# Kernel tuning notes

Measured on AMD Instinct MI355X. Metric: run time of the kernel, lower is better.

The kernel has to match this reference:

```python
import jax, jax.numpy as jnp
import numpy as np

N_SVC = 100000
N_EP = 100000
E = 300000
D = 128
H = 128


def _sage(x_src, x_dst, edge_index, Wl, bl, Wr, n_dst):
    """PyG SAGEConv default: mean neighbor aggr, lin_l(aggr) + lin_r(x_dst)."""
    src, dst = edge_index[0], edge_index[1]
    msg = x_src[src]                                        # [E, D] gather
    sums = jax.ops.segment_sum(msg, dst, num_segments=n_dst)  # [n_dst, D]
    cnt = jax.ops.segment_sum(jnp.ones((msg.shape[0], 1), msg.dtype), dst,
                              num_segments=n_dst)             # [n_dst, 1]
    mean = sums / jnp.maximum(cnt, 1.0)
    return mean @ Wl.T + bl + x_dst @ Wr.T                  # [n_dst, H]


def setup_inputs() -> dict:
    key = jax.random.key(0)
    ks = jax.random.split(key, 16)
    scale = 1.0 / np.sqrt(D)
    inp = {
        "x_service": jax.random.normal(ks[0], (N_SVC, D), jnp.float32),
        "x_endpoint": jax.random.normal(ks[1], (N_EP, D), jnp.float32),
        "ei_calls": jax.random.randint(ks[2], (2, E), 0, N_SVC),   # svc -> svc
        "ei_has": jax.random.randint(ks[3], (2, E), 0, N_SVC),     # svc -> ep (dst < N_EP too)
        "ei_belongs": jax.random.randint(ks[4], (2, E), 0, N_EP),  # ep -> svc
        "Wl_calls": jax.random.normal(ks[5], (H, D), jnp.float32) * scale,
        "bl_calls": jnp.zeros((H,), jnp.float32),
        "Wr_calls": jax.random.normal(ks[6], (H, D), jnp.float32) * scale,
        "Wl_has": jax.random.normal(ks[7], (H, D), jnp.float32) * scale,
        "bl_has": jnp.zeros((H,), jnp.float32),
        "Wr_has": jax.random.normal(ks[8], (H, D), jnp.float32) * scale,
        "Wl_belongs": jax.random.normal(ks[9], (H, D), jnp.float32) * scale,
        "bl_belongs": jnp.zeros((H,), jnp.float32),
        "Wr_belongs": jax.random.normal(ks[10], (H, D), jnp.float32) * scale,
    }
    return inp


def reference(x_service, x_endpoint, ei_calls, ei_has, ei_belongs,
              Wl_calls, bl_calls, Wr_calls,
              Wl_has, bl_has, Wr_has,
              Wl_belongs, bl_belongs, Wr_belongs):
    # edge type (service, calls, service) -> service output
    out_calls = _sage(x_service, x_service, ei_calls, Wl_calls, bl_calls, Wr_calls, N_SVC)
    # edge type (endpoint, belongs, service) -> service output
    out_belongs = _sage(x_endpoint, x_service, ei_belongs, Wl_belongs, bl_belongs, Wr_belongs, N_SVC)
    # edge type (service, has, endpoint) -> endpoint output
    out_has = _sage(x_service, x_endpoint, ei_has, Wl_has, bl_has, Wr_has, N_EP)
    # HeteroConv aggr='sum': sum per destination node type
    out_service = out_calls + out_belongs
    out_endpoint = out_has
    return out_service, out_endpoint
```

## Files before the change

kernel.cpp:

```cpp
#include <hip/hip_runtime.h>

#define DF 128
#define CAP 24

typedef __bf16 bf16x8 __attribute__((ext_vector_type(8)));
typedef float f32x4 __attribute__((ext_vector_type(4)));
typedef unsigned short ushort8v __attribute__((ext_vector_type(8)));

__device__ __forceinline__ unsigned short f2bf(float f) {
    union { float f; unsigned int u; } v; v.f = f;
    unsigned int r = v.u + 0x7FFFu + ((v.u >> 16) & 1u);
    return (unsigned short)(r >> 16);
}
__device__ __forceinline__ float bf2f(unsigned short u) {
    union { unsigned int u; float f; } v; v.u = ((unsigned int)u) << 16;
    return v.f;
}

__global__ __launch_bounds__(256)
void prep_kernel(
                 const int* __restrict__ ei_calls, int E1,
                 const int* __restrict__ ei_belongs, int E2,
                 const int* __restrict__ ei_has, int E3,
                 int* __restrict__ cnt, int* __restrict__ slots,
                 const float* __restrict__ x_service,
                 const float* __restrict__ x_endpoint,
                 unsigned short* __restrict__ A_svc,
                 unsigned short* __restrict__ A_ep,
                 int n_svc, int n_ep,
                 const float* __restrict__ Wl_calls, const float* __restrict__ Wr_calls,
                 const float* __restrict__ Wl_belongs, const float* __restrict__ Wr_belongs,
                 const float* __restrict__ Wl_has, const float* __restrict__ Wr_has,
                 const float* __restrict__ bl_calls, const float* __restrict__ bl_belongs,
                 const float* __restrict__ bl_has,
                 unsigned short* __restrict__ Bp_svc, unsigned short* __restrict__ Bp_ep,
                 float* __restrict__ bias_svc, float* __restrict__ bias_ep,
                 int B_fill, int B_pack)
{
    int b = blockIdx.x;

    if (b < B_fill) {
        int e = b * 256 + threadIdx.x;
        int Etot = E1 + E2 + E3;
        if (e >= Etot) return;
        int s, d, base;
        if (e < E1)           { s = ei_calls[e]; d = ei_calls[E1 + e]; base = 0; }
        else if (e < E1 + E2) { int el = e - E1; s = ei_belongs[el]; d = ei_belongs[E2 + el]; base = n_svc; }
        else                  { int el = e - E1 - E2; s = ei_has[el]; d = ei_has[E3 + el]; base = 2 * n_svc; }
        int g = base + d;
        int pos = atomicAdd(cnt + g, 1);
        if (pos < CAP) slots[(size_t)g * CAP + pos] = s;
        return;
    }
    b -= B_fill;

    if (b < B_pack) {
        int t = b * 256 + threadIdx.x;
        const int SV = 12 * 8 * 64 * 8;
        const int EPN = 8 * 8 * 64 * 8;
        if (t < SV) {
            int j = t & 7, lane = (t >> 3) & 63, ct = (t >> 9) & 7, kt = t >> 12;
            int k = kt * 32 + (lane >> 4) * 8 + j;
            int n = ct * 16 + (lane & 15);
            float v;
            if (k < 128)       v = Wl_calls[n * DF + k];
            else if (k < 256)  v = Wl_belongs[n * DF + (k - 128)];
            else               v = Wr_calls[n * DF + (k - 256)] + Wr_belongs[n * DF + (k - 256)];
            Bp_svc[t] = f2bf(v);
        } else if (t < SV + EPN) {
            int t2 = t - SV;
            int j = t2 & 7, lane = (t2 >> 3) & 63, ct = (t2 >> 9) & 7, kt = t2 >> 12;
            int k = kt * 32 + (lane >> 4) * 8 + j;
            int n = ct * 16 + (lane & 15);
            float v = (k < 128) ? Wl_has[n * DF + k] : Wr_has[n * DF + (k - 128)];
            Bp_ep[t2] = f2bf(v);
        }
        if (t < 128) bias_svc[t] = bl_calls[t] + bl_belongs[t];
        else if (t < 256) bias_ep[t - 128] = bl_has[t - 128];
        return;
    }
    b -= B_pack;

    int tid = b * 256 + threadIdx.x;
    int node = tid >> 5;
    int c4 = (tid & 31) << 2;
    if (node < n_svc) {
        float4 v = *reinterpret_cast<const float4*>(x_service + (size_t)node * DF + c4);
        ushort4 o; o.x = f2bf(v.x); o.y = f2bf(v.y); o.z = f2bf(v.z); o.w = f2bf(v.w);
        *reinterpret_cast<ushort4*>(A_svc + (size_t)node * 384 + 256 + c4) = o;
    } else if (node < n_svc + n_ep) {
        int ne = node - n_svc;
        float4 v = *reinterpret_cast<const float4*>(x_endpoint + (size_t)ne * DF + c4);
        ushort4 o; o.x = f2bf(v.x); o.y = f2bf(v.y); o.z = f2bf(v.z); o.w = f2bf(v.w);
        *reinterpret_cast<ushort4*>(A_ep + (size_t)ne * 256 + 128 + c4) = o;
    }
}

__global__ __launch_bounds__(256)
void aggregate_kernel(unsigned short* __restrict__ A_svc,
                      unsigned short* __restrict__ A_ep,
                      const int* __restrict__ cnt,
                      const int* __restrict__ slots,
                      int n_svc, int n_ep)
{
    int tid = blockIdx.x * blockDim.x + threadIdx.x;
    int g = tid >> 4;
    int NT = 2 * n_svc + n_ep;
    if (g >= NT) return;
    int c8 = (tid & 15) << 3;

    const unsigned short* src_base;
    size_t src_stride, src_off;
    unsigned short* outp;
    if (g < n_svc) {
        src_base = A_svc; src_stride = 384; src_off = 256;
        outp = A_svc + (size_t)g * 384 + c8;
    } else if (g < 2 * n_svc) {
        src_base = A_ep; src_stride = 256; src_off = 128;
        outp = A_svc + (size_t)(g - n_svc) * 384 + 128 + c8;
    } else {
        src_base = A_svc; src_stride = 384; src_off = 256;
        outp = A_ep + (size_t)(g - 2 * n_svc) * 256 + c8;
    }

    int deg = cnt[g];
    if (deg > CAP) deg = CAP;
    const int* sp = slots + (size_t)g * CAP;

    float acc[8];
#pragma unroll
    for (int q = 0; q < 8; ++q) acc[q] = 0.f;

    for (int i0 = 0; i0 < deg; i0 += 8) {
        int idx[8];
#pragma unroll
        for (int j = 0; j < 8; ++j) {
            int ii = i0 + j;
            if (ii > deg - 1) ii = deg - 1;
            idx[j] = sp[ii];
        }
        ushort8v v[8];
#pragma unroll
        for (int j = 0; j < 8; ++j)
            v[j] = *reinterpret_cast<const ushort8v*>(
                src_base + (size_t)idx[j] * src_stride + src_off + c8);
        int nv = deg - i0;
#pragma unroll
        for (int j = 0; j < 8; ++j) {
            if (j < nv) {
#pragma unroll
                for (int q = 0; q < 8; ++q) acc[q] += bf2f(v[j][q]);
            }
        }
    }

    float inv = 1.0f / (float)max(deg, 1);
    ushort8v o;
#pragma unroll
    for (int q = 0; q < 8; ++q) o[q] = f2bf(acc[q] * inv);
    *reinterpret_cast<ushort8v*>(outp) = o;
}

template <int KSTEPS>
__global__ __launch_bounds__(256)
void mfma_gemm(const unsigned short* __restrict__ A,
               const unsigned short* __restrict__ Bpack,
               const float* __restrict__ bias,
               float* __restrict__ out, int M)
{
    const int lane = threadIdx.x & 63;
    const int wave = threadIdx.x >> 6;
    const int quad = lane >> 4;
    const int lc = lane & 15;
    const int row0 = blockIdx.x * 128 + wave * 32;
    int m0 = row0 + lc;
    int m1 = row0 + 16 + lc;
    if (m0 > M - 1) m0 = M - 1;
    if (m1 > M - 1) m1 = M - 1;
    const int K = KSTEPS * 32;
    const unsigned short* Ap0 = A + (size_t)m0 * K + quad * 8;
    const unsigned short* Ap1 = A + (size_t)m1 * K + quad * 8;
    const unsigned short* Bp = Bpack + lane * 8;

    f32x4 acc0[8], acc1[8];
#pragma unroll
    for (int ct = 0; ct < 8; ++ct) {
        acc0[ct] = (f32x4){0.f, 0.f, 0.f, 0.f};
        acc1[ct] = (f32x4){0.f, 0.f, 0.f, 0.f};
    }

#pragma unroll
    for (int kt = 0; kt < KSTEPS; ++kt) {
        bf16x8 af0 = *reinterpret_cast<const bf16x8*>(Ap0 + kt * 32);
        bf16x8 af1 = *reinterpret_cast<const bf16x8*>(Ap1 + kt * 32);
        const unsigned short* b = Bp + (size_t)kt * 8 * 512;
#pragma unroll
        for (int ct = 0; ct < 8; ++ct) {
            bf16x8 bf = *reinterpret_cast<const bf16x8*>(b + ct * 512);
            acc0[ct] = __builtin_amdgcn_mfma_f32_16x16x32_bf16(af0, bf, acc0[ct], 0, 0, 0);
            acc1[ct] = __builtin_amdgcn_mfma_f32_16x16x32_bf16(af1, bf, acc1[ct], 0, 0, 0);
        }
    }

    float bc[8];
#pragma unroll
    for (int ct = 0; ct < 8; ++ct) bc[ct] = bias[ct * 16 + lc];

#pragma unroll
    for (int half = 0; half < 2; ++half) {
        int orow0 = row0 + half * 16 + quad * 4;
        f32x4* accp = half ? acc1 : acc0;
#pragma unroll
        for (int r = 0; r < 4; ++r) {
            int orow = orow0 + r;
            if (orow < M) {
                float* op = out + (size_t)orow * DF + lc;
#pragma unroll
                for (int ct = 0; ct < 8; ++ct) op[ct * 16] = accp[ct][r] + bc[ct];
            }
        }
    }
}

extern "C" void kernel_launch(void* const* d_in, const int* in_sizes, int n_in,
                              void* d_out, int out_size, void* d_ws, size_t ws_size,
                              hipStream_t stream)
{
    const float* x_service  = (const float*)d_in[0];
    const float* x_endpoint = (const float*)d_in[1];
    const int*   ei_calls   = (const int*)d_in[2];
    const int*   ei_has     = (const int*)d_in[3];
    const int*   ei_belongs = (const int*)d_in[4];
    const float* Wl_calls   = (const float*)d_in[5];
    const float* bl_calls   = (const float*)d_in[6];
    const float* Wr_calls   = (const float*)d_in[7];
    const float* Wl_has     = (const float*)d_in[8];
    const float* bl_has     = (const float*)d_in[9];
    const float* Wr_has     = (const float*)d_in[10];
    const float* Wl_belongs = (const float*)d_in[11];
    const float* bl_belongs = (const float*)d_in[12];
    const float* Wr_belongs = (const float*)d_in[13];

    const int n_svc = in_sizes[0] / DF;
    const int n_ep  = in_sizes[1] / DF;
    const int E1 = in_sizes[2] / 2;
    const int E3 = in_sizes[3] / 2;
    const int E2 = in_sizes[4] / 2;
    const int Etot = E1 + E2 + E3;
    const int NT = 2 * n_svc + n_ep;

    int* wsi = (int*)d_ws;
    size_t oi = 0;
    int* cnt   = wsi + oi; oi += NT;
    int* slots = wsi + oi; oi += (size_t)NT * CAP;
    oi = (oi + 3) & ~(size_t)3;

    unsigned short* wsu = (unsigned short*)(wsi + oi);
    size_t ou = 0;
    unsigned short* A_svc  = wsu + ou; ou += (size_t)n_svc * 384;
    unsigned short* A_ep   = wsu + ou; ou += (size_t)n_ep * 256;
    unsigned short* Bp_svc = wsu + ou; ou += 12 * 8 * 64 * 8;
    unsigned short* Bp_ep  = wsu + ou; ou += 8 * 8 * 64 * 8;
    ou = (ou + 7) & ~(size_t)7;
    float* bias_svc = (float*)(wsu + ou);
    float* bias_ep  = bias_svc + DF;

    hipMemsetAsync(cnt, 0, (size_t)NT * sizeof(int), stream);

    const int B_fill = (Etot + 255) / 256;
    const int B_pack = (12 * 8 * 64 * 8 + 8 * 8 * 64 * 8 + 255) / 256;
    const int B_conv = (int)(((size_t)(n_svc + n_ep) * 32 + 255) / 256);

    prep_kernel<<<B_fill + B_pack + B_conv, 256, 0, stream>>>(
        ei_calls, E1, ei_belongs, E2, ei_has, E3, cnt, slots,
        x_service, x_endpoint, A_svc, A_ep, n_svc, n_ep,
        Wl_calls, Wr_calls, Wl_belongs, Wr_belongs, Wl_has, Wr_has,
        bl_calls, bl_belongs, bl_has, Bp_svc, Bp_ep, bias_svc, bias_ep,
        B_fill, B_pack);

    aggregate_kernel<<<((size_t)NT * 16 + 255) / 256, 256, 0, stream>>>(
        A_svc, A_ep, cnt, slots, n_svc, n_ep);

    float* out_svc = (float*)d_out;
    float* out_ep  = out_svc + (size_t)n_svc * DF;

    mfma_gemm<12><<<(n_svc + 127) / 128, 256, 0, stream>>>(A_svc, Bp_svc, bias_svc, out_svc, n_svc);
    mfma_gemm<8><<<(n_ep + 127) / 128, 256, 0, stream>>>(A_ep, Bp_ep, bias_ep, out_ep, n_ep);
}
```

Baseline: 399.4 us.

## Fuse neighbor mean aggregation into GEMM via swizzled shared-memory tiles

Removes the separate aggregation kernel. Each GEMM block now gathers and averages the neighbor features for its 128 rows into an XOR-swizzled LDS tile, then runs the MFMA GEMM, reading the mean part from LDS and the self features from compact bf16 copies in global memory. This drops the write and re-read of the aggregated A matrices and one launch. In exchange the gather now runs inside the GEMM blocks with large LDS use (64KB for the service kernel), which limits occupancy and cannot overlap with the MFMA work.

Measured after the change: 414.2 us. 3.7% more time.

```diff
diff --git a/kernel.cpp b/kernel.cpp
--- a/kernel.cpp
+++ b/kernel.cpp
@@ -25,8 +25,8 @@
                  int* __restrict__ cnt, int* __restrict__ slots,
                  const float* __restrict__ x_service,
                  const float* __restrict__ x_endpoint,
-                 unsigned short* __restrict__ A_svc,
-                 unsigned short* __restrict__ A_ep,
+                 unsigned short* __restrict__ xb_svc,
+                 unsigned short* __restrict__ xb_ep,
                  int n_svc, int n_ep,
                  const float* __restrict__ Wl_calls, const float* __restrict__ Wr_calls,
                  const float* __restrict__ Wl_belongs, const float* __restrict__ Wr_belongs,
@@ -87,100 +87,109 @@
     if (node < n_svc) {
         float4 v = *reinterpret_cast<const float4*>(x_service + (size_t)node * DF + c4);
         ushort4 o; o.x = f2bf(v.x); o.y = f2bf(v.y); o.z = f2bf(v.z); o.w = f2bf(v.w);
-        *reinterpret_cast<ushort4*>(A_svc + (size_t)node * 384 + 256 + c4) = o;
+        *reinterpret_cast<ushort4*>(xb_svc + (size_t)node * DF + c4) = o;
     } else if (node < n_svc + n_ep) {
         int ne = node - n_svc;
         float4 v = *reinterpret_cast<const float4*>(x_endpoint + (size_t)ne * DF + c4);
         ushort4 o; o.x = f2bf(v.x); o.y = f2bf(v.y); o.z = f2bf(v.z); o.w = f2bf(v.w);
-        *reinterpret_cast<ushort4*>(A_ep + (size_t)ne * 256 + 128 + c4) = o;
-    }
-}
-
+        *reinterpret_cast<ushort4*>(xb_ep + (size_t)ne * DF + c4) = o;
+    }
+}
+
+template <int MODE>
 __global__ __launch_bounds__(256)
-void aggregate_kernel(unsigned short* __restrict__ A_svc,
-                      unsigned short* __restrict__ A_ep,
-                      const int* __restrict__ cnt,
-                      const int* __restrict__ slots,
-                      int n_svc, int n_ep)
+void fused_gemm(const unsigned short* __restrict__ xb_svc,
+                const unsigned short* __restrict__ xb_ep,
+                const int* __restrict__ cnt,
+                const int* __restrict__ slots,
+                const unsigned short* __restrict__ Bpack,
+                const float* __restrict__ bias,
+                float* __restrict__ out,
+                int n_svc, int n_ep)
 {
-    int tid = blockIdx.x * blockDim.x + threadIdx.x;
-    int g = tid >> 4;
-    int NT = 2 * n_svc + n_ep;
-    if (g >= NT) return;
-    int c8 = (tid & 15) << 3;
-
-    const unsigned short* src_base;
-    size_t src_stride, src_off;
-    unsigned short* outp;
-    if (g < n_svc) {
-        src_base = A_svc; src_stride = 384; src_off = 256;
-        outp = A_svc + (size_t)g * 384 + c8;
-    } else if (g < 2 * n_svc) {
-        src_base = A_ep; src_stride = 256; src_off = 128;
-        outp = A_svc + (size_t)(g - n_svc) * 384 + 128 + c8;
-    } else {
-        src_base = A_svc; src_stride = 384; src_off = 256;
-        outp = A_ep + (size_t)(g - 2 * n_svc) * 256 + c8;
-    }
-
-    int deg = cnt[g];
-    if (deg > CAP) deg = CAP;
-    const int* sp = slots + (size_t)g * CAP;
-
-    float acc[8];
-#pragma unroll
-    for (int q = 0; q < 8; ++q) acc[q] = 0.f;
-
-    for (int i0 = 0; i0 < deg; i0 += 8) {
-        int idx[8];
-#pragma unroll
-        for (int j = 0; j < 8; ++j) {
-            int ii = i0 + j;
-            if (ii > deg - 1) ii = deg - 1;
-            idx[j] = sp[ii];
-        }
-        ushort8v v[8];
-#pragma unroll
-        for (int j = 0; j < 8; ++j)
-            v[j] = *reinterpret_cast<const ushort8v*>(
-                src_base + (size_t)idx[j] * src_stride + src_off + c8);
-        int nv = deg - i0;
-#pragma unroll
-        for (int j = 0; j < 8; ++j) {
-            if (j < nv) {
-#pragma unroll
-                for (int q = 0; q < 8; ++q) acc[q] += bf2f(v[j][q]);
+    constexpr int MK      = (MODE == 0) ? 256 : 128;
+    constexpr int KSTEPS  = (MODE == 0) ? 12 : 8;
+    constexpr int MKSTEPS = MK / 32;
+    constexpr int NG      = (MODE == 0) ? 256 : 128;
+
+    __shared__ unsigned short smean[128 * MK];
+
+    const int M = (MODE == 0) ? n_svc : n_ep;
+    const int row_base = blockIdx.x * 128;
+
+#pragma unroll 1
+    for (int it = 0; it < NG * 16 / 256; ++it) {
+        int task   = it * 256 + threadIdx.x;
+        int gl     = task >> 4;
+        int lane16 = task & 15;
+        int node   = gl & 127;
+        int t      = gl >> 7;
+        int chunk  = lane16 + t * 16;
+        unsigned short* dst = smean + node * MK + ((chunk ^ (node & 7)) << 3);
+
+        int gnode = row_base + node;
+        float acc[8];
+#pragma unroll
+        for (int q = 0; q < 8; ++q) acc[q] = 0.f;
+        int deg = 0;
+        if (gnode < M) {
+            int g;
+            const unsigned short* src;
+            if (MODE == 0) {
+                g   = (t == 0) ? gnode : (n_svc + gnode);
+                src = (t == 0) ? xb_svc : xb_ep;
+            } else {
+                g   = 2 * n_svc + gnode;
+                src = xb_svc;
             }
-        }
-    }
-
-    float inv = 1.0f / (float)max(deg, 1);
-    ushort8v o;
-#pragma unroll
-    for (int q = 0; q < 8; ++q) o[q] = f2bf(acc[q] * inv);
-    *reinterpret_cast<ushort8v*>(outp) = o;
-}
-
-template <int KSTEPS>
-__global__ __launch_bounds__(256)
-void mfma_gemm(const unsigned short* __restrict__ A,
-               const unsigned short* __restrict__ Bpack,
-               const float* __restrict__ bias,
-               float* __restrict__ out, int M)
-{
+            deg = cnt[g];
+            if (deg > CAP) deg = CAP;
+            const int* sp = slots + (size_t)g * CAP;
+            int c8 = lane16 << 3;
+            for (int i0 = 0; i0 < deg; i0 += 8) {
+                int idx[8];
+#pragma unroll
+                for (int j = 0; j < 8; ++j) {
+                    int ii = i0 + j;
+                    if (ii > deg - 1) ii = deg - 1;
+                    idx[j] = sp[ii];
+                }
+                ushort8v v[8];
+#pragma unroll
+                for (int j = 0; j < 8; ++j)
+                    v[j] = *reinterpret_cast<const ushort8v*>(
+                        src + (size_t)idx[j] * DF + c8);
+                int nv = deg - i0;
+#pragma unroll
+                for (int j = 0; j < 8; ++j) {
+                    if (j < nv) {
+#pragma unroll
+                        for (int q = 0; q < 8; ++q) acc[q] += bf2f(v[j][q]);
+                    }
+                }
+            }
+        }
+        float inv = 1.0f / (float)max(deg, 1);
+        ushort8v o;
+#pragma unroll
+        for (int q = 0; q < 8; ++q) o[q] = f2bf(acc[q] * inv);
+        *reinterpret_cast<ushort8v*>(dst) = o;
+    }
+    __syncthreads();
+
     const int lane = threadIdx.x & 63;
     const int wave = threadIdx.x >> 6;
     const int quad = lane >> 4;
-    const int lc = lane & 15;
-    const int row0 = blockIdx.x * 128 + wave * 32;
-    int m0 = row0 + lc;
-    int m1 = row0 + 16 + lc;
-    if (m0 > M - 1) m0 = M - 1;
-    if (m1 > M - 1) m1 = M - 1;
-    const int K = KSTEPS * 32;
-    const unsigned short* Ap0 = A + (size_t)m0 * K + quad * 8;
-    const unsigned short* Ap1 = A + (size_t)m1 * K + quad * 8;
-    const unsigned short* Bp = Bpack + lane * 8;
+    const int lc   = lane & 15;
+    const int m0l  = wave * 32 + lc;
+    const int m1l  = m0l + 16;
+    int m0 = row_base + m0l; if (m0 > M - 1) m0 = M - 1;
+    int m1 = row_base + m1l; if (m1 > M - 1) m1 = M - 1;
+
+    const unsigned short* xb_dst = (MODE == 0) ? xb_svc : xb_ep;
+    const unsigned short* Xp0 = xb_dst + (size_t)m0 * DF + quad * 8;
+    const unsigned short* Xp1 = xb_dst + (size_t)m1 * DF + quad * 8;
+    const unsigned short* Bp  = Bpack + lane * 8;
 
     f32x4 acc0[8], acc1[8];
 #pragma unroll
@@ -191,12 +200,21 @@
 
 #pragma unroll
     for (int kt = 0; kt < KSTEPS; ++kt) {
-        bf16x8 af0 = *reinterpret_cast<const bf16x8*>(Ap0 + kt * 32);
-        bf16x8 af1 = *reinterpret_cast<const bf16x8*>(Ap1 + kt * 32);
-        const unsigned short* b = Bp + (size_t)kt * 8 * 512;
+        bf16x8 af0, af1;
+        if (kt < MKSTEPS) {
+            int c = kt * 4 + quad;
+            af0 = *reinterpret_cast<const bf16x8*>(
+                smean + m0l * MK + ((c ^ (m0l & 7)) << 3));
+            af1 = *reinterpret_cast<const bf16x8*>(
+                smean + m1l * MK + ((c ^ (m1l & 7)) << 3));
+        } else {
+            af0 = *reinterpret_cast<const bf16x8*>(Xp0 + (kt - MKSTEPS) * 32);
+            af1 = *reinterpret_cast<const bf16x8*>(Xp1 + (kt - MKSTEPS) * 32);
+        }
+        const unsigned short* bptr = Bp + (size_t)kt * 8 * 512;
 #pragma unroll
         for (int ct = 0; ct < 8; ++ct) {
-            bf16x8 bf = *reinterpret_cast<const bf16x8*>(b + ct * 512);
+            bf16x8 bf = *reinterpret_cast<const bf16x8*>(bptr + ct * 512);
             acc0[ct] = __builtin_amdgcn_mfma_f32_16x16x32_bf16(af0, bf, acc0[ct], 0, 0, 0);
             acc1[ct] = __builtin_amdgcn_mfma_f32_16x16x32_bf16(af1, bf, acc1[ct], 0, 0, 0);
         }
@@ -206,6 +224,7 @@
 #pragma unroll
     for (int ct = 0; ct < 8; ++ct) bc[ct] = bias[ct * 16 + lc];
 
+    const int row0 = row_base + wave * 32;
 #pragma unroll
     for (int half = 0; half < 2; ++half) {
         int orow0 = row0 + half * 16 + quad * 4;
@@ -257,8 +276,8 @@
 
     unsigned short* wsu = (unsigned short*)(wsi + oi);
     size_t ou = 0;
-    unsigned short* A_svc  = wsu + ou; ou += (size_t)n_svc * 384;
-    unsigned short* A_ep   = wsu + ou; ou += (size_t)n_ep * 256;
+    unsigned short* xb_svc = wsu + ou; ou += (size_t)n_svc * DF;
+    unsigned short* xb_ep  = wsu + ou; ou += (size_t)n_ep * DF;
     unsigned short* Bp_svc = wsu + ou; ou += 12 * 8 * 64 * 8;
     unsigned short* Bp_ep  = wsu + ou; ou += 8 * 8 * 64 * 8;
     ou = (ou + 7) & ~(size_t)7;
@@ -273,17 +292,16 @@
 
     prep_kernel<<<B_fill + B_pack + B_conv, 256, 0, stream>>>(
         ei_calls, E1, ei_belongs, E2, ei_has, E3, cnt, slots,
-        x_service, x_endpoint, A_svc, A_ep, n_svc, n_ep,
+        x_service, x_endpoint, xb_svc, xb_ep, n_svc, n_ep,
         Wl_calls, Wr_calls, Wl_belongs, Wr_belongs, Wl_has, Wr_has,
         bl_calls, bl_belongs, bl_has, Bp_svc, Bp_ep, bias_svc, bias_ep,
         B_fill, B_pack);
 
-    aggregate_kernel<<<((size_t)NT * 16 + 255) / 256, 256, 0, stream>>>(
-        A_svc, A_ep, cnt, slots, n_svc, n_ep);
-
     float* out_svc = (float*)d_out;
     float* out_ep  = out_svc + (size_t)n_svc * DF;
 
-    mfma_gemm<12><<<(n_svc + 127) / 128, 256, 0, stream>>>(A_svc, Bp_svc, bias_svc, out_svc, n_svc);
-    mfma_gemm<8><<<(n_ep + 127) / 128, 256, 0, stream>>>(A_ep, Bp_ep, bias_ep, out_ep, n_ep);
-}
+    fused_gemm<0><<<(n_svc + 127) / 128, 256, 0, stream>>>(
+        xb_svc, xb_ep, cnt, slots, Bp_svc, bias_svc, out_svc, n_svc, n_ep);
+    fused_gemm<1><<<(n_ep + 127) / 128, 256, 0, stream>>>(
+        xb_svc, xb_ep, cnt, slots, Bp_ep, bias_ep, out_ep, n_svc, n_ep);
+}
```
